# Performance work log

Hardware: AMD Instinct MI355X
Metric: run time of the kernel (lower is better)

## Reference

```python
import jax, jax.numpy as jnp
import numpy as np

COS_EPS = 1e-6   # torch CosineSimilarity eps
NORM_EPS = 1e-10 # assignment-normalizer eps


def setup_inputs() -> dict:
    key = jax.random.key(0)
    ks = jax.random.split(key, 12)
    s = 0.1
    H, K, Din, Dout = 8, 128, 64, 64
    return {
        "node_set": jax.random.normal(ks[0], (32, Din, 1024, 12), jnp.float32),
        "adj": jax.random.uniform(ks[1], (32, 1024, 1024), jnp.float32),
        "W0": jax.random.normal(ks[2], (Din, Din), jnp.float32) * s,
        "w_i2c": jax.random.normal(ks[3], (H, 1), jnp.float32) * s,
        "b_i2c": jax.random.normal(ks[4], (H,), jnp.float32) * s,
        "W_lin": jax.random.normal(ks[5], (H * K, H), jnp.float32) * s,
        "b_lin": jax.random.normal(ks[6], (H * K,), jnp.float32) * s,
        "conv_w": jax.random.normal(ks[7], (H,), jnp.float32) * s,
        "conv_b": jax.random.normal(ks[8], (), jnp.float32) * s,
        "W_feat": jax.random.normal(ks[9], (Dout, Din), jnp.float32) * s,
        "b_feat": jax.random.normal(ks[10], (Dout,), jnp.float32) * s,
    }


def reference(node_set, adj, W0, w_i2c, b_i2c, W_lin, b_lin, conv_w, conv_b, W_feat, b_feat):
    # [B, C, N, T] -> [B, N, C, T] -> mean over T -> [B, N, D]
    x = jnp.mean(jnp.transpose(node_set, (0, 2, 1, 3)), axis=3)
    B = x.shape[0]
    H = w_i2c.shape[0]
    K = W_lin.shape[0] // H

    # get_att: attention-pooled global centroid seed [B, 1, D]
    temp = jnp.mean(x, axis=1, keepdims=True)                 # [B,1,D]
    h_avg = jnp.tanh(jnp.einsum('bod,de->boe', temp, W0))    # [B,1,D]
    att = jnp.einsum('bnd,bod->bno', x, h_avg)               # [B,N,1]
    cent = jnp.einsum('bno,bnd->bod', att, x)                # [B,1,D]

    # generate batch centroids: [B,D,1] -> [B,D,H] -> [B,D,H*K] -> [B,H,K,D]
    bc = jnp.transpose(cent, (0, 2, 1))                       # [B,D,1]
    bc = jax.nn.relu(bc @ w_i2c.T + b_i2c)                    # [B,D,H]
    bc = jax.nn.relu(bc @ W_lin.T + b_lin)                    # [B,D,H*K]
    bc = jnp.transpose(bc, (0, 2, 1)).reshape(B, H, K, -1)    # [B,H,K,D]

    # cosine-similarity assignment (no 5D repeat: dot / max(|x||c|, eps))
    dots = jnp.einsum('bnd,bhkd->bhkn', x, bc)                # [B,H,K,N]
    xn = jnp.linalg.norm(x, axis=-1)                          # [B,N]
    cn = jnp.linalg.norm(bc, axis=-1)                         # [B,H,K]
    C_heads = dots / jnp.maximum(cn[..., None] * xn[:, None, None, :], COS_EPS)
    # normalize over centroids dim (dim 2)
    C_heads = C_heads / (jnp.sum(C_heads, axis=2, keepdims=True) + NORM_EPS)

    # 1x1 conv over heads -> single assignment matrix [B,K,N]
    C = jnp.einsum('h,bhkn->bkn', conv_w, C_heads) + conv_b

    # pooled node features + output projection
    new_node_set = jnp.einsum('bkn,bnd->bkd', C, x)           # [B,K,D]
    return new_node_set @ W_feat.T + b_feat                   # [B,K,Dout]
```

## Files before the change

kernel.cpp:

```cpp
#include <hip/hip_runtime.h>
#include <math.h>

#define B_  32
#define N_  1024
#define D_  64
#define H_  8
#define K_  128
#define HK_ 1024
#define T_  12

__global__ __launch_bounds__(256) void k1_mean(const float* __restrict__ ns,
        float* __restrict__ x, float* __restrict__ invxn,
        float* __restrict__ tempsum) {
    __shared__ float tile[64][65];
    int b    = blockIdx.x >> 4;
    int n0   = (blockIdx.x & 15) << 6;
    int lane = threadIdx.x & 63;
    int w    = threadIdx.x >> 6;
    #pragma unroll
    for (int j = 0; j < 16; ++j) {
        int d = w * 16 + j;
        const float4* p = (const float4*)(ns +
            ((size_t)((b * 64 + d) * 1024 + n0 + lane)) * 12);
        float4 a = p[0], c = p[1], e = p[2];
        float s = ((a.x + a.y) + (a.z + a.w)) + ((c.x + c.y) + (c.z + c.w))
                + ((e.x + e.y) + (e.z + e.w));
        tile[lane][d] = s * (1.0f / 12.0f);
    }
    __syncthreads();
    #pragma unroll
    for (int j = 0; j < 16; ++j) {
        int r = w * 16 + j;
        x[((size_t)(b * 1024 + n0 + r)) * 64 + lane] = tile[r][lane];
    }
    #pragma unroll
    for (int j = 0; j < 16; ++j) {
        int r = w * 16 + j;
        float v  = tile[r][lane];
        float ss = v * v;
        #pragma unroll
        for (int o = 32; o; o >>= 1) ss += __shfl_xor(ss, o);
        if (lane == 0) invxn[b * 1024 + n0 + r] = 1.0f / sqrtf(fmaxf(ss, 1e-30f));
    }
    if (threadIdx.x < 64) {
        float s = 0.0f;
        #pragma unroll 8
        for (int r = 0; r < 64; ++r) s += tile[r][threadIdx.x];
        atomicAdd(&tempsum[b * 64 + threadIdx.x], s);
    }
}

__global__ void k2_havg(const float* __restrict__ tempsum,
        const float* __restrict__ W0, float* __restrict__ h_avg) {
    __shared__ float t[64];
    int b = blockIdx.x, e = threadIdx.x;
    t[e] = tempsum[b * 64 + e] * (1.0f / 1024.0f);
    __syncthreads();
    float a = 0.0f;
    #pragma unroll 8
    for (int d = 0; d < 64; ++d) a += t[d] * W0[d * 64 + e];
    h_avg[b * 64 + e] = tanhf(a);
}

__global__ __launch_bounds__(256) void k3_cent(const float* __restrict__ x,
        const float* __restrict__ h_avg, float* __restrict__ cent) {
    __shared__ float ha[64];
    __shared__ float cp[4][64];
    int b    = blockIdx.x >> 3;
    int n0   = (blockIdx.x & 7) << 7;
    int lane = threadIdx.x & 63;
    int w    = threadIdx.x >> 6;
    if (threadIdx.x < 64) ha[threadIdx.x] = h_avg[b * 64 + threadIdx.x];
    __syncthreads();
    float hv = ha[lane];
    float cw = 0.0f;
    for (int nn = w; nn < 128; nn += 4) {
        float xv = x[((size_t)(b * 1024 + n0 + nn)) * 64 + lane];
        float d  = xv * hv;
        #pragma unroll
        for (int o = 32; o; o >>= 1) d += __shfl_xor(d, o);
        cw += d * xv;
    }
    cp[w][lane] = cw;
    __syncthreads();
    if (w == 0)
        atomicAdd(&cent[b * 64 + lane],
                  cp[0][lane] + cp[1][lane] + cp[2][lane] + cp[3][lane]);
}

__global__ __launch_bounds__(256) void k4_bc(const float* __restrict__ cent,
        const float* __restrict__ w_i2c, const float* __restrict__ b_i2c,
        const float* __restrict__ W_lin, const float* __restrict__ b_lin,
        float* __restrict__ bc, float* __restrict__ invcn) {
    int lane = threadIdx.x & 63;
    int w    = threadIdx.x >> 6;
    int g    = blockIdx.x * 4 + w;
    int b    = g >> 10, kk = g & 1023;
    float c   = cent[b * 64 + lane];
    float pre = b_lin[kk];
    #pragma unroll
    for (int h = 0; h < 8; ++h) {
        float b1 = fmaxf(c * w_i2c[h] + b_i2c[h], 0.0f);
        pre += b1 * W_lin[kk * 8 + h];
    }
    float v = fmaxf(pre, 0.0f);
    bc[((size_t)g) * 64 + lane] = v;
    float ss = v * v;
    #pragma unroll
    for (int o = 32; o; o >>= 1) ss += __shfl_xor(ss, o);
    if (lane == 0) invcn[g] = (ss > 0.0f) ? (1.0f / sqrtf(ss)) : 0.0f;
}

__global__ __launch_bounds__(256, 1) void k5_assign(const float* __restrict__ x,
        const float* __restrict__ bc, const float* __restrict__ invxn,
        const float* __restrict__ invcn, const float* __restrict__ conv_w,
        const float* __restrict__ conv_b, float* __restrict__ C) {
    __shared__ float xt[128][68];
    __shared__ float bct[128][68];
    __shared__ float invx_s[128];
    __shared__ float invc_s[128];
    __shared__ float sred[16][132];
    __shared__ float sinv[128];
    int b   = blockIdx.x >> 3;
    int n0  = (blockIdx.x & 7) << 7;
    int tid = threadIdx.x;
    {
        int r = tid >> 1, dh = (tid & 1) << 5;
        const float4* src = (const float4*)(x + ((size_t)(b * 1024 + n0 + r)) * 64 + dh);
        float4* dst = (float4*)(&xt[r][dh]);
        #pragma unroll
        for (int qq = 0; qq < 8; ++qq) dst[qq] = src[qq];
    }
    if (tid < 128) invx_s[tid] = invxn[b * 1024 + n0 + tid];
    float Cacc[8][8];
    #pragma unroll
    for (int i = 0; i < 8; ++i)
        #pragma unroll
        for (int j = 0; j < 8; ++j) Cacc[i][j] = 0.0f;
    int q = tid >> 4, p = tid & 15;
    float cb = conv_b[0];
    for (int h = 0; h < 8; ++h) {
        {
            int r = tid >> 1, dh = (tid & 1) << 5;
            const float4* src = (const float4*)(bc + ((size_t)(b * 1024 + h * 128 + r)) * 64 + dh);
            float4* dst = (float4*)(&bct[r][dh]);
            #pragma unroll
            for (int qq = 0; qq < 8; ++qq) dst[qq] = src[qq];
        }
        if (tid < 128) invc_s[tid] = invcn[b * 1024 + h * 128 + tid];
        __syncthreads();
        float acc[8][8];
        #pragma unroll
        for (int i = 0; i < 8; ++i)
            #pragma unroll
            for (int j = 0; j < 8; ++j) acc[i][j] = 0.0f;
        for (int dc = 0; dc < 64; dc += 4) {
            float4 bv[8], xv[8];
            #pragma unroll
            for (int i = 0; i < 8; ++i) bv[i] = *(const float4*)(&bct[q + 16 * i][dc]);
            #pragma unroll
            for (int j = 0; j < 8; ++j) xv[j] = *(const float4*)(&xt[p + 16 * j][dc]);
            #pragma unroll
            for (int i = 0; i < 8; ++i)
                #pragma unroll
                for (int j = 0; j < 8; ++j)
                    acc[i][j] += bv[i].x * xv[j].x + bv[i].y * xv[j].y
                               + bv[i].z * xv[j].z + bv[i].w * xv[j].w;
        }
        float part[8];
        #pragma unroll
        for (int j = 0; j < 8; ++j) part[j] = 0.0f;
        #pragma unroll
        for (int i = 0; i < 8; ++i) {
            float ic = invc_s[q + 16 * i];
            #pragma unroll
            for (int j = 0; j < 8; ++j) {
                float v = acc[i][j] * ic * invx_s[p + 16 * j];
                acc[i][j] = v;
                part[j] += v;
            }
        }
        #pragma unroll
        for (int j = 0; j < 8; ++j) sred[q][p + 16 * j] = part[j];
        __syncthreads();
        if (tid < 128) {
            float s = 0.0f;
            #pragma unroll
            for (int qq = 0; qq < 16; ++qq) s += sred[qq][tid];
            sinv[tid] = 1.0f / (s + 1e-10f);
        }
        __syncthreads();
        float cwv = conv_w[h];
        #pragma unroll
        for (int j = 0; j < 8; ++j) {
            float si = sinv[p + 16 * j];
            #pragma unroll
            for (int i = 0; i < 8; ++i) Cacc[i][j] += cwv * acc[i][j] * si;
        }
        __syncthreads();
    }
    #pragma unroll
    for (int i = 0; i < 8; ++i) {
        int k = q + 16 * i;
        #pragma unroll
        for (int j = 0; j < 8; ++j)
            C[((size_t)(b * 128 + k)) * 1024 + n0 + p + 16 * j] = Cacc[i][j] + cb;
    }
}

__global__ __launch_bounds__(256) void k6_out(const float* __restrict__ C,
        const float* __restrict__ x, const float* __restrict__ W_feat,
        const float* __restrict__ b_feat, float* __restrict__ out) {
    __shared__ float wf[64][65];
    __shared__ float nns[16][65];
    int b    = blockIdx.x >> 3;
    int k0   = (blockIdx.x & 7) << 4;
    int lane = threadIdx.x & 63;
    int w    = threadIdx.x >> 6;
    for (int t = threadIdx.x; t < 4096; t += 256) wf[t >> 6][t & 63] = W_feat[t];
    float acc0 = 0, acc1 = 0, acc2 = 0, acc3 = 0;
    const float* xb = x + ((size_t)b << 16);
    const float* Cb = C + (((size_t)(b * 128 + k0 + w * 4)) << 10);
    #pragma unroll 4
    for (int n = 0; n < 1024; ++n) {
        float xv = xb[n * 64 + lane];
        acc0 += Cb[n]        * xv;
        acc1 += Cb[1024 + n] * xv;
        acc2 += Cb[2048 + n] * xv;
        acc3 += Cb[3072 + n] * xv;
    }
    nns[w * 4 + 0][lane] = acc0;
    nns[w * 4 + 1][lane] = acc1;
    nns[w * 4 + 2][lane] = acc2;
    nns[w * 4 + 3][lane] = acc3;
    __syncthreads();
    float bf = b_feat[lane];
    #pragma unroll
    for (int m = 0; m < 4; ++m) {
        float a = bf;
        #pragma unroll 8
        for (int d = 0; d < 64; ++d) a += nns[w * 4 + m][d] * wf[lane][d];
        out[((size_t)(b * 128 + k0 + w * 4 + m)) * 64 + lane] = a;
    }
}

extern "C" void kernel_launch(void* const* d_in, const int* in_sizes, int n_in,
                              void* d_out, int out_size, void* d_ws, size_t ws_size,
                              hipStream_t stream) {
    const float* node_set = (const float*)d_in[0];
    const float* W0     = (const float*)d_in[2];
    const float* w_i2c  = (const float*)d_in[3];
    const float* b_i2c  = (const float*)d_in[4];
    const float* W_lin  = (const float*)d_in[5];
    const float* b_lin  = (const float*)d_in[6];
    const float* conv_w = (const float*)d_in[7];
    const float* conv_b = (const float*)d_in[8];
    const float* W_feat = (const float*)d_in[9];
    const float* b_feat = (const float*)d_in[10];
    float* out = (float*)d_out;
    float* ws  = (float*)d_ws;

    float* x       = ws;
    float* invxn   = ws + 2097152;
    float* tempsum = ws + 2129920;
    float* cent    = ws + 2131968;
    float* h_avg   = ws + 2134016;
    float* bc      = ws + 2136064;
    float* invcn   = ws + 4233216;
    float* Cmat    = ws + 4265984;

    hipMemsetAsync(tempsum, 0, 4096 * sizeof(float), stream);

    k1_mean <<<B_ * 16, 256, 0, stream>>>(node_set, x, invxn, tempsum);
    k2_havg <<<B_, 64, 0, stream>>>(tempsum, W0, h_avg);
    k3_cent <<<B_ * 8, 256, 0, stream>>>(x, h_avg, cent);
    k4_bc   <<<B_ * HK_ / 4, 256, 0, stream>>>(cent, w_i2c, b_i2c, W_lin, b_lin, bc, invcn);
    k5_assign<<<B_ * 8, 256, 0, stream>>>(x, bc, invxn, invcn, conv_w, conv_b, Cmat);
    k6_out  <<<B_ * 8, 256, 0, stream>>>(Cmat, x, W_feat, b_feat, out);
}
```

Before: 459.9 us.

## Fuse havg into centroid kernel, retile assignment and output kernels for occupancy

Merges the h_avg computation into the centroid kernel, removing one launch. Doubles thread count in the mean kernel and block count in centroid and assignment kernels, with the assignment kernel using 64-node tiles and allowing two blocks per CU. The basis-centroid kernel computes four rows per wave to reuse the first-layer activations. The output kernel now stages C and x tiles through shared memory instead of per-lane strided global reads, which adds more synchronisation.

```diff
diff --git a/kernel.cpp b/kernel.cpp
--- a/kernel.cpp
+++ b/kernel.cpp
@@ -7,9 +7,8 @@
 #define H_  8
 #define K_  128
 #define HK_ 1024
-#define T_  12
-
-__global__ __launch_bounds__(256) void k1_mean(const float* __restrict__ ns,
+
+__global__ __launch_bounds__(512) void k1_mean(const float* __restrict__ ns,
         float* __restrict__ x, float* __restrict__ invxn,
         float* __restrict__ tempsum) {
     __shared__ float tile[64][65];
@@ -18,8 +17,8 @@
     int lane = threadIdx.x & 63;
     int w    = threadIdx.x >> 6;
     #pragma unroll
-    for (int j = 0; j < 16; ++j) {
-        int d = w * 16 + j;
+    for (int j = 0; j < 8; ++j) {
+        int d = w * 8 + j;
         const float4* p = (const float4*)(ns +
             ((size_t)((b * 64 + d) * 1024 + n0 + lane)) * 12);
         float4 a = p[0], c = p[1], e = p[2];
@@ -29,14 +28,10 @@
     }
     __syncthreads();
     #pragma unroll
-    for (int j = 0; j < 16; ++j) {
-        int r = w * 16 + j;
-        x[((size_t)(b * 1024 + n0 + r)) * 64 + lane] = tile[r][lane];
-    }
-    #pragma unroll
-    for (int j = 0; j < 16; ++j) {
-        int r = w * 16 + j;
-        float v  = tile[r][lane];
+    for (int j = 0; j < 8; ++j) {
+        int r = w * 8 + j;
+        float v = tile[r][lane];
+        x[((size_t)(b * 1024 + n0 + r)) * 64 + lane] = v;
         float ss = v * v;
         #pragma unroll
         for (int o = 32; o; o >>= 1) ss += __shfl_xor(ss, o);
@@ -44,37 +39,34 @@
     }
     if (threadIdx.x < 64) {
         float s = 0.0f;
-        #pragma unroll 8
+        #pragma unroll 16
         for (int r = 0; r < 64; ++r) s += tile[r][threadIdx.x];
         atomicAdd(&tempsum[b * 64 + threadIdx.x], s);
     }
 }
 
-__global__ void k2_havg(const float* __restrict__ tempsum,
-        const float* __restrict__ W0, float* __restrict__ h_avg) {
+__global__ __launch_bounds__(256) void k3_cent(const float* __restrict__ x,
+        const float* __restrict__ tempsum, const float* __restrict__ W0,
+        float* __restrict__ cent) {
     __shared__ float t[64];
-    int b = blockIdx.x, e = threadIdx.x;
-    t[e] = tempsum[b * 64 + e] * (1.0f / 1024.0f);
-    __syncthreads();
-    float a = 0.0f;
-    #pragma unroll 8
-    for (int d = 0; d < 64; ++d) a += t[d] * W0[d * 64 + e];
-    h_avg[b * 64 + e] = tanhf(a);
-}
-
-__global__ __launch_bounds__(256) void k3_cent(const float* __restrict__ x,
-        const float* __restrict__ h_avg, float* __restrict__ cent) {
     __shared__ float ha[64];
     __shared__ float cp[4][64];
-    int b    = blockIdx.x >> 3;
-    int n0   = (blockIdx.x & 7) << 7;
+    int b    = blockIdx.x >> 4;
+    int n0   = (blockIdx.x & 15) << 6;
     int lane = threadIdx.x & 63;
     int w    = threadIdx.x >> 6;
-    if (threadIdx.x < 64) ha[threadIdx.x] = h_avg[b * 64 + threadIdx.x];
+    if (threadIdx.x < 64) t[threadIdx.x] = tempsum[b * 64 + threadIdx.x] * (1.0f / 1024.0f);
+    __syncthreads();
+    if (threadIdx.x < 64) {
+        float a = 0.0f;
+        #pragma unroll 8
+        for (int d = 0; d < 64; ++d) a += t[d] * W0[d * 64 + threadIdx.x];
+        ha[threadIdx.x] = tanhf(a);
+    }
     __syncthreads();
     float hv = ha[lane];
     float cw = 0.0f;
-    for (int nn = w; nn < 128; nn += 4) {
+    for (int nn = w; nn < 64; nn += 4) {
         float xv = x[((size_t)(b * 1024 + n0 + nn)) * 64 + lane];
         float d  = xv * hv;
         #pragma unroll
@@ -94,49 +86,53 @@
         float* __restrict__ bc, float* __restrict__ invcn) {
     int lane = threadIdx.x & 63;
     int w    = threadIdx.x >> 6;
-    int g    = blockIdx.x * 4 + w;
-    int b    = g >> 10, kk = g & 1023;
-    float c   = cent[b * 64 + lane];
-    float pre = b_lin[kk];
-    #pragma unroll
-    for (int h = 0; h < 8; ++h) {
-        float b1 = fmaxf(c * w_i2c[h] + b_i2c[h], 0.0f);
-        pre += b1 * W_lin[kk * 8 + h];
-    }
-    float v = fmaxf(pre, 0.0f);
-    bc[((size_t)g) * 64 + lane] = v;
-    float ss = v * v;
-    #pragma unroll
-    for (int o = 32; o; o >>= 1) ss += __shfl_xor(ss, o);
-    if (lane == 0) invcn[g] = (ss > 0.0f) ? (1.0f / sqrtf(ss)) : 0.0f;
-}
-
-__global__ __launch_bounds__(256, 1) void k5_assign(const float* __restrict__ x,
+    int gg   = blockIdx.x * 4 + w;
+    int b    = gg >> 8;
+    int kk0  = (gg & 255) * 4;
+    float c = cent[b * 64 + lane];
+    float b1[8];
+    #pragma unroll
+    for (int h = 0; h < 8; ++h) b1[h] = fmaxf(c * w_i2c[h] + b_i2c[h], 0.0f);
+    #pragma unroll
+    for (int u = 0; u < 4; ++u) {
+        int kk = kk0 + u;
+        float pre = b_lin[kk];
+        #pragma unroll
+        for (int h = 0; h < 8; ++h) pre += b1[h] * W_lin[kk * 8 + h];
+        float v = fmaxf(pre, 0.0f);
+        bc[((size_t)(b * 1024 + kk)) * 64 + lane] = v;
+        float ss = v * v;
+        #pragma unroll
+        for (int o = 32; o; o >>= 1) ss += __shfl_xor(ss, o);
+        if (lane == 0) invcn[b * 1024 + kk] = (ss > 0.0f) ? (1.0f / sqrtf(ss)) : 0.0f;
+    }
+}
+
+__global__ __launch_bounds__(256, 2) void k5_assign(const float* __restrict__ x,
         const float* __restrict__ bc, const float* __restrict__ invxn,
         const float* __restrict__ invcn, const float* __restrict__ conv_w,
         const float* __restrict__ conv_b, float* __restrict__ C) {
-    __shared__ float xt[128][68];
+    __shared__ float xt[64][68];
     __shared__ float bct[128][68];
-    __shared__ float invx_s[128];
+    __shared__ float invx_s[64];
     __shared__ float invc_s[128];
-    __shared__ float sred[16][132];
-    __shared__ float sinv[128];
-    int b   = blockIdx.x >> 3;
-    int n0  = (blockIdx.x & 7) << 7;
+    __shared__ float sred[16][68];
+    __shared__ float sinv[64];
+    int b   = blockIdx.x >> 4;
+    int n0  = (blockIdx.x & 15) << 6;
     int tid = threadIdx.x;
     {
-        int r = tid >> 1, dh = (tid & 1) << 5;
+        int r = tid >> 2, dh = (tid & 3) << 4;
         const float4* src = (const float4*)(x + ((size_t)(b * 1024 + n0 + r)) * 64 + dh);
         float4* dst = (float4*)(&xt[r][dh]);
-        #pragma unroll
-        for (int qq = 0; qq < 8; ++qq) dst[qq] = src[qq];
-    }
-    if (tid < 128) invx_s[tid] = invxn[b * 1024 + n0 + tid];
-    float Cacc[8][8];
+        dst[0] = src[0]; dst[1] = src[1]; dst[2] = src[2]; dst[3] = src[3];
+    }
+    if (tid < 64) invx_s[tid] = invxn[b * 1024 + n0 + tid];
+    float Cacc[8][4];
     #pragma unroll
     for (int i = 0; i < 8; ++i)
         #pragma unroll
-        for (int j = 0; j < 8; ++j) Cacc[i][j] = 0.0f;
+        for (int j = 0; j < 4; ++j) Cacc[i][j] = 0.0f;
     int q = tid >> 4, p = tid & 15;
     float cb = conv_b[0];
     for (int h = 0; h < 8; ++h) {
@@ -145,45 +141,45 @@
             const float4* src = (const float4*)(bc + ((size_t)(b * 1024 + h * 128 + r)) * 64 + dh);
             float4* dst = (float4*)(&bct[r][dh]);
             #pragma unroll
-            for (int qq = 0; qq < 8; ++qq) dst[qq] = src[qq];
+            for (int u = 0; u < 8; ++u) dst[u] = src[u];
         }
         if (tid < 128) invc_s[tid] = invcn[b * 1024 + h * 128 + tid];
         __syncthreads();
-        float acc[8][8];
+        float acc[8][4];
         #pragma unroll
         for (int i = 0; i < 8; ++i)
             #pragma unroll
-            for (int j = 0; j < 8; ++j) acc[i][j] = 0.0f;
+            for (int j = 0; j < 4; ++j) acc[i][j] = 0.0f;
         for (int dc = 0; dc < 64; dc += 4) {
-            float4 bv[8], xv[8];
+            float4 bv[8], xv[4];
             #pragma unroll
             for (int i = 0; i < 8; ++i) bv[i] = *(const float4*)(&bct[q + 16 * i][dc]);
             #pragma unroll
-            for (int j = 0; j < 8; ++j) xv[j] = *(const float4*)(&xt[p + 16 * j][dc]);
+            for (int j = 0; j < 4; ++j) xv[j] = *(const float4*)(&xt[p + 16 * j][dc]);
             #pragma unroll
             for (int i = 0; i < 8; ++i)
                 #pragma unroll
-                for (int j = 0; j < 8; ++j)
+                for (int j = 0; j < 4; ++j)
                     acc[i][j] += bv[i].x * xv[j].x + bv[i].y * xv[j].y
                                + bv[i].z * xv[j].z + bv[i].w * xv[j].w;
         }
-        float part[8];
-        #pragma unroll
-        for (int j = 0; j < 8; ++j) part[j] = 0.0f;
+        float part[4];
+        #pragma unroll
+        for (int j = 0; j < 4; ++j) part[j] = 0.0f;
         #pragma unroll
         for (int i = 0; i < 8; ++i) {
             float ic = invc_s[q + 16 * i];
             #pragma unroll
-            for (int j = 0; j < 8; ++j) {
+            for (int j = 0; j < 4; ++j) {
                 float v = acc[i][j] * ic * invx_s[p + 16 * j];
                 acc[i][j] = v;
                 part[j] += v;
             }
         }
         #pragma unroll
-        for (int j = 0; j < 8; ++j) sred[q][p + 16 * j] = part[j];
-        __syncthreads();
-        if (tid < 128) {
+        for (int j = 0; j < 4; ++j) sred[q][p + 16 * j] = part[j];
+        __syncthreads();
+        if (tid < 64) {
             float s = 0.0f;
             #pragma unroll
             for (int qq = 0; qq < 16; ++qq) s += sred[qq][tid];
@@ -192,7 +188,7 @@
         __syncthreads();
         float cwv = conv_w[h];
         #pragma unroll
-        for (int j = 0; j < 8; ++j) {
+        for (int j = 0; j < 4; ++j) {
             float si = sinv[p + 16 * j];
             #pragma unroll
             for (int i = 0; i < 8; ++i) Cacc[i][j] += cwv * acc[i][j] * si;
@@ -203,45 +199,66 @@
     for (int i = 0; i < 8; ++i) {
         int k = q + 16 * i;
         #pragma unroll
-        for (int j = 0; j < 8; ++j)
+        for (int j = 0; j < 4; ++j)
             C[((size_t)(b * 128 + k)) * 1024 + n0 + p + 16 * j] = Cacc[i][j] + cb;
     }
 }
 
-__global__ __launch_bounds__(256) void k6_out(const float* __restrict__ C,
-        const float* __restrict__ x, const float* __restrict__ W_feat,
-        const float* __restrict__ b_feat, float* __restrict__ out) {
-    __shared__ float wf[64][65];
-    __shared__ float nns[16][65];
-    int b    = blockIdx.x >> 3;
-    int k0   = (blockIdx.x & 7) << 4;
-    int lane = threadIdx.x & 63;
-    int w    = threadIdx.x >> 6;
-    for (int t = threadIdx.x; t < 4096; t += 256) wf[t >> 6][t & 63] = W_feat[t];
-    float acc0 = 0, acc1 = 0, acc2 = 0, acc3 = 0;
-    const float* xb = x + ((size_t)b << 16);
-    const float* Cb = C + (((size_t)(b * 128 + k0 + w * 4)) << 10);
-    #pragma unroll 4
-    for (int n = 0; n < 1024; ++n) {
-        float xv = xb[n * 64 + lane];
-        acc0 += Cb[n]        * xv;
-        acc1 += Cb[1024 + n] * xv;
-        acc2 += Cb[2048 + n] * xv;
-        acc3 += Cb[3072 + n] * xv;
-    }
-    nns[w * 4 + 0][lane] = acc0;
-    nns[w * 4 + 1][lane] = acc1;
-    nns[w * 4 + 2][lane] = acc2;
-    nns[w * 4 + 3][lane] = acc3;
-    __syncthreads();
-    float bf = b_feat[lane];
-    #pragma unroll
-    for (int m = 0; m < 4; ++m) {
-        float a = bf;
+__global__ __launch_bounds__(256, 2) void k6_out(const float* __restrict__ C,
+        const float* __restrict__ x, const float* __restrict__ Wf,
+        const float* __restrict__ bfeat, float* __restrict__ out) {
+    __shared__ float xt[128][68];
+    __shared__ float ct[16][132];
+    __shared__ float nnst[16][68];
+    __shared__ float wfs[64][68];
+    int b   = blockIdx.x >> 3;
+    int k0  = (blockIdx.x & 7) << 4;
+    int tid = threadIdx.x;
+    int kq  = tid >> 4, p = tid & 15;
+    for (int t = tid; t < 4096; t += 256) wfs[t >> 6][t & 63] = Wf[t];
+    float acc[4] = {0.0f, 0.0f, 0.0f, 0.0f};
+    for (int c = 0; c < 8; ++c) {
+        __syncthreads();
+        {
+            int r = tid >> 1, dh = (tid & 1) << 5;
+            const float4* src = (const float4*)(x + ((size_t)(b * 1024 + c * 128 + r)) * 64 + dh);
+            float4* dst = (float4*)(&xt[r][dh]);
+            #pragma unroll
+            for (int u = 0; u < 8; ++u) dst[u] = src[u];
+        }
+        for (int t = tid; t < 2048; t += 256)
+            ct[t >> 7][t & 127] = C[((size_t)(b * 128 + k0 + (t >> 7))) * 1024 + c * 128 + (t & 127)];
+        __syncthreads();
         #pragma unroll 8
-        for (int d = 0; d < 64; ++d) a += nns[w * 4 + m][d] * wf[lane][d];
-        out[((size_t)(b * 128 + k0 + w * 4 + m)) * 64 + lane] = a;
-    }
+        for (int n = 0; n < 128; ++n) {
+            float  cv = ct[kq][n];
+            float4 xv = *(const float4*)(&xt[n][p << 2]);
+            acc[0] += cv * xv.x; acc[1] += cv * xv.y;
+            acc[2] += cv * xv.z; acc[3] += cv * xv.w;
+        }
+    }
+    __syncthreads();
+    nnst[kq][(p << 2) + 0] = acc[0];
+    nnst[kq][(p << 2) + 1] = acc[1];
+    nnst[kq][(p << 2) + 2] = acc[2];
+    nnst[kq][(p << 2) + 3] = acc[3];
+    __syncthreads();
+    float o0 = bfeat[(p << 2) + 0], o1 = bfeat[(p << 2) + 1];
+    float o2 = bfeat[(p << 2) + 2], o3 = bfeat[(p << 2) + 3];
+    #pragma unroll
+    for (int dc = 0; dc < 64; dc += 4) {
+        float4 nv = *(const float4*)(&nnst[kq][dc]);
+        float4 w0 = *(const float4*)(&wfs[(p << 2) + 0][dc]);
+        float4 w1 = *(const float4*)(&wfs[(p << 2) + 1][dc]);
+        float4 w2 = *(const float4*)(&wfs[(p << 2) + 2][dc]);
+        float4 w3 = *(const float4*)(&wfs[(p << 2) + 3][dc]);
+        o0 += nv.x * w0.x + nv.y * w0.y + nv.z * w0.z + nv.w * w0.w;
+        o1 += nv.x * w1.x + nv.y * w1.y + nv.z * w1.z + nv.w * w1.w;
+        o2 += nv.x * w2.x + nv.y * w2.y + nv.z * w2.z + nv.w * w2.w;
+        o3 += nv.x * w3.x + nv.y * w3.y + nv.z * w3.z + nv.w * w3.w;
+    }
+    float4 ov = make_float4(o0, o1, o2, o3);
+    *(float4*)(out + ((size_t)(b * 128 + k0 + kq)) * 64 + (p << 2)) = ov;
 }
 
 extern "C" void kernel_launch(void* const* d_in, const int* in_sizes, int n_in,
@@ -264,17 +281,15 @@
     float* invxn   = ws + 2097152;
     float* tempsum = ws + 2129920;
     float* cent    = ws + 2131968;
-    float* h_avg   = ws + 2134016;
-    float* bc      = ws + 2136064;
-    float* invcn   = ws + 4233216;
-    float* Cmat    = ws + 4265984;
+    float* bc      = ws + 2134016;
+    float* invcn   = ws + 4231168;
+    float* Cmat    = ws + 4263936;
 
     hipMemsetAsync(tempsum, 0, 4096 * sizeof(float), stream);
 
-    k1_mean <<<B_ * 16, 256, 0, stream>>>(node_set, x, invxn, tempsum);
-    k2_havg <<<B_, 64, 0, stream>>>(tempsum, W0, h_avg);
-    k3_cent <<<B_ * 8, 256, 0, stream>>>(x, h_avg, cent);
-    k4_bc   <<<B_ * HK_ / 4, 256, 0, stream>>>(cent, w_i2c, b_i2c, W_lin, b_lin, bc, invcn);
-    k5_assign<<<B_ * 8, 256, 0, stream>>>(x, bc, invxn, invcn, conv_w, conv_b, Cmat);
-    k6_out  <<<B_ * 8, 256, 0, stream>>>(Cmat, x, W_feat, b_feat, out);
-}
+    k1_mean  <<<B_ * 16, 512, 0, stream>>>(node_set, x, invxn, tempsum);
+    k3_cent  <<<B_ * 16, 256, 0, stream>>>(x, tempsum, W0, cent);
+    k4_bc    <<<2048,    256, 0, stream>>>(cent, w_i2c, b_i2c, W_lin, b_lin, bc, invcn);
+    k5_assign<<<B_ * 16, 256, 0, stream>>>(x, bc, invxn, invcn, conv_w, conv_b, Cmat);
+    k6_out   <<<B_ * 8,  256, 0, stream>>>(Cmat, x, W_feat, b_feat, out);
+}
```

Measured after the change: 379.4 us. -17.5%, faster.
